# Kernel optimization log

Measured on AMD Instinct MI355X. Metric: run time of the kernel, lower is better.

Reference implementation:

```python
import jax, jax.numpy as jnp
import numpy as np

D, H, L, MLP = 1024, 16, 4, 4096
DH = D // H
EPS = 1e-5
SCALE_BASE = 512.0  # rotary_embedding_torch xpos default

def _ln(x, w, b):
    m = jnp.mean(x, axis=-1, keepdims=True)
    v = jnp.mean((x - m) ** 2, axis=-1, keepdims=True)
    return (x - m) * jax.lax.rsqrt(v + EPS) * w + b

def _rotate_half(x):
    # interleaved pair rotation: (x0, x1) -> (-x1, x0)
    x1, x2 = x[..., 0::2], x[..., 1::2]
    return jnp.stack((-x2, x1), axis=-1).reshape(x.shape)

def _rope_tables(S):
    inv = 1.0 / (10000.0 ** (jnp.arange(0, DH, 2, dtype=jnp.float32) / DH))
    pos = jnp.arange(S, dtype=jnp.float32)
    freqs = jnp.repeat(pos[:, None] * inv[None, :], 2, axis=-1)      # [S, DH]
    base = (jnp.arange(0, DH, 2, dtype=jnp.float32) + 0.4 * DH) / (1.4 * DH)
    power = (pos - S // 2) / SCALE_BASE
    scale = jnp.repeat(base[None, :] ** power[:, None], 2, axis=-1)  # [S, DH] xpos scale
    return jnp.cos(freqs), jnp.sin(freqs), scale

def setup_inputs() -> dict:
    key = jax.random.key(0)
    ks = jax.random.split(key, 8)
    B, S = 4, 1024
    w = 0.02
    return {
        "x": jax.random.normal(ks[0], (B, S, D), jnp.float32),
        "ln1_w": jnp.ones((L, D), jnp.float32), "ln1_b": jnp.zeros((L, D), jnp.float32),
        "wqkv": jax.random.normal(ks[1], (L, D, 3 * D), jnp.float32) * w,
        "bqkv": jnp.zeros((L, 3 * D), jnp.float32),
        "wo": jax.random.normal(ks[2], (L, D, D), jnp.float32) * w,
        "bo": jnp.zeros((L, D), jnp.float32),
        "ln2_w": jnp.ones((L, D), jnp.float32), "ln2_b": jnp.zeros((L, D), jnp.float32),
        "w1": jax.random.normal(ks[3], (L, D, MLP), jnp.float32) * w,
        "b1": jnp.zeros((L, MLP), jnp.float32),
        "w2": jax.random.normal(ks[4], (L, D, MLP), jnp.float32) * w,
        "b2": jnp.zeros((L, MLP), jnp.float32),
        "wout": jax.random.normal(ks[5], (L, MLP, D), jnp.float32) * w,
        "bout": jnp.zeros((L, D), jnp.float32),
        "fln_w": jnp.ones((D,), jnp.float32), "fln_b": jnp.zeros((D,), jnp.float32),
    }

def reference(x, ln1_w, ln1_b, wqkv, bqkv, wo, bo, ln2_w, ln2_b,
              w1, b1, w2, b2, wout, bout, fln_w, fln_b):
    B, S, _ = x.shape
    cos, sin, scale = _rope_tables(S)
    cos, sin, scale = cos[:, None, :], sin[:, None, :], scale[:, None, :]  # [S,1,DH] bcast heads
    inv_scale = 1.0 / scale
    attn_scale = DH ** -0.5
    for l in range(L):
        normed = _ln(x, ln1_w[l], ln1_b[l])
        qkv = (normed @ wqkv[l] + bqkv[l]).reshape(B, S, 3, H, DH)
        q, k, v = qkv[:, :, 0], qkv[:, :, 1], qkv[:, :, 2]  # [B,S,H,DH]
        q = (q * cos + _rotate_half(q) * sin) * scale       # xpos rotary, queries
        k = (k * cos + _rotate_half(k) * sin) * inv_scale   # xpos rotary, keys (scale**-1)
        attn = jnp.einsum('bihd,bjhd->bhij', q, k) * attn_scale
        attn = jax.nn.softmax(attn, axis=-1)
        y = jnp.einsum('bhij,bjhd->bihd', attn, v).reshape(B, S, D)
        x = x + y @ wo[l] + bo[l]
        h = _ln(x, ln2_w[l], ln2_b[l])
        ff = (jax.nn.silu(h @ w1[l] + b1[l]) * (h @ w2[l] + b2[l])) @ wout[l] + bout[l]
        x = x + ff
    return _ln(x, fln_w, fln_b)
```

## Files before the change

### kernel.cpp

```cpp
#include <hip/hip_runtime.h>
#include <hip/hip_bf16.h>
#include <math.h>


#define TD 1024
#define TH 16
#define TDH 64
#define TL 4
#define TMLP 4096
#define TB 4
#define TS 1024
#define TM (TB*TS)

typedef __attribute__((ext_vector_type(8))) short short8;
typedef __attribute__((ext_vector_type(4))) float f32x4;
typedef __attribute__((ext_vector_type(4))) unsigned short us4;
typedef __attribute__((ext_vector_type(2))) unsigned short us2;

__device__ __forceinline__ float bf2f(unsigned short u) {
  union { unsigned int i; float f; } x; x.i = ((unsigned int)u) << 16; return x.f;
}
__device__ __forceinline__ unsigned short f2bf(float f) {
  unsigned int x = __float_as_uint(f);
  unsigned int r = (x + 0x7FFFu + ((x >> 16) & 1u)) >> 16;
  return (unsigned short)r;
}

#if defined(__has_builtin)
#if __has_builtin(__builtin_amdgcn_global_load_lds)
#define TE_HAS_GLL 1
#endif
#endif

__device__ __forceinline__ void stage16(void* lds, const void* g) {
#ifdef TE_HAS_GLL
  __builtin_amdgcn_global_load_lds(
      (const __attribute__((address_space(1))) void*)g,
      (__attribute__((address_space(3))) void*)lds, 16, 0, 0);
#else
  *(short8*)lds = *(const short8*)g;
#endif
}

#define MFMA_BF16(a,b,c) __builtin_amdgcn_mfma_f32_16x16x32_bf16((a),(b),(c),0,0,0)

__global__ __launch_bounds__(256)
void te_tab(float4* __restrict__ tab) {
  int idx = blockIdx.x * 256 + threadIdx.x;
  int s = idx >> 5, i = idx & 31;
  float inv = powf(10000.0f, -(2.0f * (float)i) / 64.0f);
  float fr = (float)s * inv;
  float c = cosf(fr), sn = sinf(fr);
  float base = (2.0f * (float)i + 0.4f * 64.0f) / (1.4f * 64.0f);
  float p = ((float)s - 512.0f) / 512.0f;
  float scl = powf(base, p);
  float4 t;
  t.x = c; t.y = sn; t.z = scl * 0.125f; t.w = 1.0f / scl;
  tab[idx] = t;
}

__global__ __launch_bounds__(256)
void te_transpose_cvt(const float* __restrict__ src, unsigned short* __restrict__ dst,
                      int K, int N) {
  __shared__ float tile[32][33];
  int n0 = blockIdx.x * 32, k0 = blockIdx.y * 32;
  int tx = threadIdx.x, ty = threadIdx.y;
  #pragma unroll
  for (int j = 0; j < 4; ++j)
    tile[ty + 8*j][tx] = src[(size_t)(k0 + ty + 8*j) * N + n0 + tx];
  __syncthreads();
  #pragma unroll
  for (int j = 0; j < 4; ++j)
    dst[(size_t)(n0 + ty + 8*j) * K + k0 + tx] = f2bf(tile[tx][ty + 8*j]);
}

template<int OUTBF>
__global__ __launch_bounds__(256)
void te_ln(const float* __restrict__ in, const float* __restrict__ w,
           const float* __restrict__ b, void* __restrict__ outp) {
  int row = blockIdx.x, t = threadIdx.x;
  float4 v = ((const float4*)(in + (size_t)row * TD))[t];
  float s = v.x + v.y + v.z + v.w;
  float sq = v.x*v.x + v.y*v.y + v.z*v.z + v.w*v.w;
  #pragma unroll
  for (int o = 1; o < 64; o <<= 1) { s += __shfl_xor(s, o); sq += __shfl_xor(sq, o); }
  __shared__ float red[8];
  int wv = t >> 6;
  if ((t & 63) == 0) { red[wv] = s; red[4 + wv] = sq; }
  __syncthreads();
  s  = red[0] + red[1] + red[2] + red[3];
  sq = red[4] + red[5] + red[6] + red[7];
  float mean = s * (1.0f / TD);
  float rstd = rsqrtf(sq * (1.0f / TD) - mean * mean + 1e-5f);
  float4 w4 = ((const float4*)w)[t];
  float4 b4 = ((const float4*)b)[t];
  float r0 = (v.x - mean) * rstd * w4.x + b4.x;
  float r1 = (v.y - mean) * rstd * w4.y + b4.y;
  float r2 = (v.z - mean) * rstd * w4.z + b4.z;
  float r3 = (v.w - mean) * rstd * w4.w + b4.w;
  if (OUTBF) {
    us4 pk; pk[0] = f2bf(r0); pk[1] = f2bf(r1); pk[2] = f2bf(r2); pk[3] = f2bf(r3);
    ((us4*)outp)[(size_t)row * (TD/4) + t] = pk;
  } else {
    float4 o; o.x = r0; o.y = r1; o.z = r2; o.w = r3;
    ((float4*)outp)[(size_t)row * (TD/4) + t] = o;
  }
}

template<int MODE>
__global__ __launch_bounds__(256)
void te_gemm(const unsigned short* __restrict__ A, const unsigned short* __restrict__ Bt,
             const float* __restrict__ bias, const float* resid,
             const unsigned short* __restrict__ gate, void* outp,
             int M, int N, int K) {
  __shared__ short As[2][128 * 64];
  __shared__ short Bs[2][128 * 64];
  int bm = blockIdx.x, bn = blockIdx.y;
  int t = threadIdx.x;
  int lane = t & 63, w = t >> 6;
  int wr = w >> 1, wc = w & 1;
  int lr = lane & 15, lk = lane >> 4;
  f32x4 acc[4][4] = {};

  const short* Abase = (const short*)A + (size_t)(bm * 128) * K;
  const short* Bbase = (const short*)Bt + (size_t)(bn * 128) * K;
  int srow[4], scol[4];
  #pragma unroll
  for (int j = 0; j < 4; ++j) {
    int m = j * 256 + t;
    int r = m >> 3, c = m & 7;
    srow[j] = r;
    scol[j] = (c ^ (r & 7)) * 8;
  }

  auto stage_tile = [&](int buf, int k0) {
    #pragma unroll
    for (int j = 0; j < 4; ++j) {
      stage16(&As[buf][j * 2048 + t * 8], Abase + (size_t)srow[j] * K + k0 + scol[j]);
      stage16(&Bs[buf][j * 2048 + t * 8], Bbase + (size_t)srow[j] * K + k0 + scol[j]);
    }
  };

  auto compute_tile = [&](int buf) {
    #pragma unroll
    for (int ks = 0; ks < 2; ++ks) {
      short8 af[4], bfv[4];
      #pragma unroll
      for (int mi = 0; mi < 4; ++mi) {
        int row = wr * 64 + mi * 16 + lr;
        int cc = (ks * 4 + lk) ^ (row & 7);
        af[mi] = *(const short8*)&As[buf][row * 64 + cc * 8];
      }
      #pragma unroll
      for (int nj = 0; nj < 4; ++nj) {
        int row = wc * 64 + nj * 16 + lr;
        int cc = (ks * 4 + lk) ^ (row & 7);
        bfv[nj] = *(const short8*)&Bs[buf][row * 64 + cc * 8];
      }
      #pragma unroll
      for (int mi = 0; mi < 4; ++mi)
        #pragma unroll
        for (int nj = 0; nj < 4; ++nj)
          acc[mi][nj] = MFMA_BF16(af[mi], bfv[nj], acc[mi][nj]);
    }
  };

  int nk = K >> 6;
  stage_tile(0, 0);
  __syncthreads();
  int cur = 0;
  for (int kt = 0; kt < nk; ++kt) {
    if (kt + 1 < nk) stage_tile(cur ^ 1, (kt + 1) << 6);
    compute_tile(cur);
    __syncthreads();
    cur ^= 1;
  }

  #pragma unroll
  for (int mi = 0; mi < 4; ++mi) {
    #pragma unroll
    for (int nj = 0; nj < 4; ++nj) {
      int col = bn*128 + wc*64 + nj*16 + lr;
      float bv = bias[col];
      #pragma unroll
      for (int r = 0; r < 4; ++r) {
        int row = bm*128 + wr*64 + mi*16 + lk*4 + r;
        size_t o = (size_t)row * N + col;
        float val = acc[mi][nj][r] + bv;
        if (MODE == 0) {
          ((unsigned short*)outp)[o] = f2bf(val);
        } else if (MODE == 1) {
          ((float*)outp)[o] = resid[o] + val;
        } else {
          float a = bf2f(gate[o]);
          float sg = a / (1.0f + __expf(-a));
          ((unsigned short*)outp)[o] = f2bf(sg * val);
        }
      }
    }
  }
}

__global__ __launch_bounds__(256)
void te_rope(const unsigned short* __restrict__ qkv, const float4* __restrict__ tab,
             unsigned short* __restrict__ qb, unsigned short* __restrict__ kb) {
  int idx = blockIdx.x * 256 + threadIdx.x;
  int i = idx & 31;
  int h = (idx >> 5) & 15;
  int row = idx >> 9;
  int s = row & (TS - 1);
  float4 t4 = tab[(s << 5) + i];
  size_t base = (size_t)row * (3*TD) + h * TDH + 2*i;
  us2 qp = *(const us2*)&qkv[base];
  us2 kp = *(const us2*)&qkv[base + TD];
  float qe = bf2f(qp[0]), qo = bf2f(qp[1]);
  float ke = bf2f(kp[0]), ko = bf2f(kp[1]);
  size_t ob = (size_t)row * TD + h * TDH + 2*i;
  us2 qo2, ko2;
  qo2[0] = f2bf((qe * t4.x - qo * t4.y) * t4.z);
  qo2[1] = f2bf((qo * t4.x + qe * t4.y) * t4.z);
  ko2[0] = f2bf((ke * t4.x - ko * t4.y) * t4.w);
  ko2[1] = f2bf((ko * t4.x + ke * t4.y) * t4.w);
  *(us2*)&qb[ob] = qo2;
  *(us2*)&kb[ob] = ko2;
}

__global__ __launch_bounds__(256)
void te_attn(const unsigned short* __restrict__ qb, const unsigned short* __restrict__ kb,
             const unsigned short* __restrict__ qkv, unsigned short* __restrict__ y) {
  __shared__ char Ks[8192];
  __shared__ char Vs[8192];
  __shared__ char Ps[4][2048];
  int qt = blockIdx.x;
  int bh = blockIdx.y;
  int b = bh >> 4, h = bh & 15;
  int t = threadIdx.x, lane = t & 63, w = t >> 6;
  int lq = lane & 15, lg = lane >> 4;

  const unsigned short* vptr = qkv + 2*TD;

  int qrow = b*TS + qt*64 + w*16 + lq;
  short8 aq0 = *(const short8*)&qb[(size_t)qrow*TD + h*TDH + lg*8];
  short8 aq1 = *(const short8*)&qb[(size_t)qrow*TD + h*TDH + 32 + lg*8];

  f32x4 oacc[4] = {};
  float rm[4] = {-3e38f, -3e38f, -3e38f, -3e38f};
  float rl[4] = {0.f, 0.f, 0.f, 0.f};

  int srr = t >> 3;
  int scb = (t & 7) * 8;

  for (int kt = 0; kt < TS/64; ++kt) {
    int kbase = b*TS + kt*64;
    __syncthreads();
    #pragma unroll
    for (int half = 0; half < 2; ++half) {
      int row = srr + half*32;
      short8 d = *(const short8*)&kb[(size_t)(kbase + row)*TD + h*TDH + scb];
      int off = (row*128 + scb*2) ^ ((row & 7) << 4);
      *(short8*)&Ks[off] = d;
    }
    #pragma unroll
    for (int half = 0; half < 2; ++half) {
      int dh = srr + half*32;
      short8 d;
      #pragma unroll
      for (int i = 0; i < 8; ++i)
        d[i] = (short)vptr[(size_t)(kbase + scb + i)*(3*TD) + h*TDH + dh];
      int off = (dh*128 + scb*2) ^ ((dh & 7) << 4);
      *(short8*)&Vs[off] = d;
    }
    __syncthreads();
    f32x4 sc[4];
    #pragma unroll
    for (int nj = 0; nj < 4; ++nj) {
      int row = nj*16 + lq;
      int sw = (row & 7) << 4;
      short8 b0 = *(const short8*)&Ks[(row*128 + lg*16) ^ sw];
      short8 b1 = *(const short8*)&Ks[(row*128 + 64 + lg*16) ^ sw];
      f32x4 c = {};
      c = MFMA_BF16(aq0, b0, c);
      c = MFMA_BF16(aq1, b1, c);
      sc[nj] = c;
    }
    float mn[4], al[4];
    #pragma unroll
    for (int r = 0; r < 4; ++r) {
      float x = fmaxf(fmaxf(sc[0][r], sc[1][r]), fmaxf(sc[2][r], sc[3][r]));
      #pragma unroll
      for (int o = 1; o < 16; o <<= 1) x = fmaxf(x, __shfl_xor(x, o));
      mn[r] = fmaxf(rm[r], x);
      al[r] = __expf(rm[r] - mn[r]);
      rm[r] = mn[r];
    }
    #pragma unroll
    for (int nj = 0; nj < 4; ++nj)
      #pragma unroll
      for (int r = 0; r < 4; ++r)
        sc[nj][r] = __expf(sc[nj][r] - mn[r]);
    #pragma unroll
    for (int r = 0; r < 4; ++r) {
      float x = sc[0][r] + sc[1][r] + sc[2][r] + sc[3][r];
      #pragma unroll
      for (int o = 1; o < 16; o <<= 1) x += __shfl_xor(x, o);
      rl[r] = rl[r] * al[r] + x;
    }
    #pragma unroll
    for (int d0 = 0; d0 < 4; ++d0)
      #pragma unroll
      for (int r = 0; r < 4; ++r)
        oacc[d0][r] *= al[r];
    #pragma unroll
    for (int nj = 0; nj < 4; ++nj)
      #pragma unroll
      for (int r = 0; r < 4; ++r) {
        int row = lg*4 + r;
        int off = (row*128 + (nj*16 + lq)*2) ^ ((row & 7) << 4);
        *(short*)&Ps[w][off] = (short)f2bf(sc[nj][r]);
      }
    short8 pa0, pa1;
    {
      int sw = (lq & 7) << 4;
      pa0 = *(const short8*)&Ps[w][(lq*128 + lg*16) ^ sw];
      pa1 = *(const short8*)&Ps[w][(lq*128 + 64 + lg*16) ^ sw];
    }
    #pragma unroll
    for (int d0 = 0; d0 < 4; ++d0) {
      int row = d0*16 + lq;
      int sw = (row & 7) << 4;
      short8 b0 = *(const short8*)&Vs[(row*128 + lg*16) ^ sw];
      short8 b1 = *(const short8*)&Vs[(row*128 + 64 + lg*16) ^ sw];
      oacc[d0] = MFMA_BF16(pa0, b0, oacc[d0]);
      oacc[d0] = MFMA_BF16(pa1, b1, oacc[d0]);
    }
  }
  #pragma unroll
  for (int d0 = 0; d0 < 4; ++d0)
    #pragma unroll
    for (int r = 0; r < 4; ++r) {
      int row = b*TS + qt*64 + w*16 + lg*4 + r;
      float val = oacc[d0][r] / rl[r];
      y[(size_t)row*TD + h*TDH + d0*16 + lq] = f2bf(val);
    }
}

extern "C" void kernel_launch(void* const* d_in, const int* in_sizes, int n_in,
                              void* d_out, int out_size, void* d_ws, size_t ws_size,
                              hipStream_t stream) {
  const float* x_in = (const float*)d_in[0];
  const float* ln1w = (const float*)d_in[1];
  const float* ln1b = (const float*)d_in[2];
  const float* wqkv = (const float*)d_in[3];
  const float* bqkv = (const float*)d_in[4];
  const float* wo   = (const float*)d_in[5];
  const float* bo   = (const float*)d_in[6];
  const float* ln2w = (const float*)d_in[7];
  const float* ln2b = (const float*)d_in[8];
  const float* w1   = (const float*)d_in[9];
  const float* b1   = (const float*)d_in[10];
  const float* w2   = (const float*)d_in[11];
  const float* b2   = (const float*)d_in[12];
  const float* wout = (const float*)d_in[13];
  const float* bout = (const float*)d_in[14];
  const float* flnw = (const float*)d_in[15];
  const float* flnb = (const float*)d_in[16];

  char* ws = (char*)d_ws;
  size_t off = 0;
  auto alloc = [&](size_t bytes) -> void* {
    void* p = ws + off;
    off += (bytes + 255) & ~(size_t)255;
    return p;
  };
  unsigned short* wqkv_t = (unsigned short*)alloc((size_t)3*TD*TD*2);
  unsigned short* wo_t   = (unsigned short*)alloc((size_t)TD*TD*2);
  unsigned short* w1_t   = (unsigned short*)alloc((size_t)TMLP*TD*2);
  unsigned short* w2_t   = (unsigned short*)alloc((size_t)TMLP*TD*2);
  unsigned short* wout_t = (unsigned short*)alloc((size_t)TD*TMLP*2);
  float*          x      = (float*)alloc((size_t)TM*TD*4);
  unsigned short* nrm    = (unsigned short*)alloc((size_t)TM*TD*2);
  unsigned short* u1     = (unsigned short*)alloc((size_t)TM*TMLP*2);
  unsigned short* qbuf   = (unsigned short*)alloc((size_t)TM*TD*2);
  unsigned short* kbuf   = (unsigned short*)alloc((size_t)TM*TD*2);
  unsigned short* u2     = (unsigned short*)alloc((size_t)TM*TMLP*2);
  float4*         tab    = (float4*)alloc((size_t)TS*32*sizeof(float4));

  dim3 blk256(256);
  dim3 tblk(32, 8);
  te_tab<<<dim3(TS*32/256), blk256, 0, stream>>>(tab);
  hipMemcpyAsync(x, x_in, (size_t)TM*TD*4, hipMemcpyDeviceToDevice, stream);

  for (int l = 0; l < TL; ++l) {
    te_transpose_cvt<<<dim3(3*TD/32, TD/32), tblk, 0, stream>>>(
        wqkv + (size_t)l*TD*3*TD, wqkv_t, TD, 3*TD);
    te_transpose_cvt<<<dim3(TD/32, TD/32), tblk, 0, stream>>>(
        wo + (size_t)l*TD*TD, wo_t, TD, TD);
    te_transpose_cvt<<<dim3(TMLP/32, TD/32), tblk, 0, stream>>>(
        w1 + (size_t)l*TD*TMLP, w1_t, TD, TMLP);
    te_transpose_cvt<<<dim3(TMLP/32, TD/32), tblk, 0, stream>>>(
        w2 + (size_t)l*TD*TMLP, w2_t, TD, TMLP);
    te_transpose_cvt<<<dim3(TD/32, TMLP/32), tblk, 0, stream>>>(
        wout + (size_t)l*TMLP*TD, wout_t, TMLP, TD);

    te_ln<1><<<dim3(TM), blk256, 0, stream>>>(x, ln1w + l*TD, ln1b + l*TD, nrm);
    te_gemm<0><<<dim3(TM/128, 3*TD/128), blk256, 0, stream>>>(
        nrm, wqkv_t, bqkv + l*3*TD, nullptr, nullptr, u1, TM, 3*TD, TD);
    te_rope<<<dim3(TM*TH*32/256), blk256, 0, stream>>>(u1, tab, qbuf, kbuf);
    te_attn<<<dim3(TS/64, TB*TH), blk256, 0, stream>>>(qbuf, kbuf, u1, u2);
    te_gemm<1><<<dim3(TM/128, TD/128), blk256, 0, stream>>>(
        u2, wo_t, bo + l*TD, x, nullptr, x, TM, TD, TD);
    te_ln<1><<<dim3(TM), blk256, 0, stream>>>(x, ln2w + l*TD, ln2b + l*TD, nrm);
    te_gemm<0><<<dim3(TM/128, TMLP/128), blk256, 0, stream>>>(
        nrm, w1_t, b1 + l*TMLP, nullptr, nullptr, u1, TM, TMLP, TD);
    te_gemm<2><<<dim3(TM/128, TMLP/128), blk256, 0, stream>>>(
        nrm, w2_t, b2 + l*TMLP, nullptr, u1, u2, TM, TMLP, TD);
    te_gemm<1><<<dim3(TM/128, TD/128), blk256, 0, stream>>>(
        u2, wout_t, bout + l*TD, x, nullptr, x, TM, TD, TMLP);
  }
  te_ln<0><<<dim3(TM), blk256, 0, stream>>>(x, flnw, flnb, (float*)d_out);

  (void)in_sizes; (void)n_in; (void)out_size; (void)ws_size;
}
```

Measured before the change: 1.726 ms.

## Fuse gated MLP GEMMs, pre-transpose V, pipeline attention K/V loads, use exp2

Interleaves w1 and w2 weights into one transposed buffer so a single 256x256-tile, 512-thread GEMM computes both projections and applies SiLU gating in its epilogue. This removes the separate u1 write and re-read and the second pass over the normalized activations. V is transposed into a per-head buffer by a new kernel, so attention can load K and V with double-buffered async LDS staging instead of strided scalar gathers. Attention blocks are remapped to group heads per XCD, and softmax uses exp2 with log2(e) folded into the query scale. The cost is an extra transpose kernel, plus higher LDS and register pressure in the larger GEMM tile.

```diff
diff --git a/kernel.cpp b/kernel.cpp
--- a/kernel.cpp
+++ b/kernel.cpp
@@ -11,6 +11,8 @@
 #define TB 4
 #define TS 1024
 #define TM (TB*TS)
+
+#define LOG2E 1.4426950408889634f
 
 typedef __attribute__((ext_vector_type(8))) short short8;
 typedef __attribute__((ext_vector_type(4))) float f32x4;
@@ -55,7 +57,7 @@
   float p = ((float)s - 512.0f) / 512.0f;
   float scl = powf(base, p);
   float4 t;
-  t.x = c; t.y = sn; t.z = scl * 0.125f; t.w = 1.0f / scl;
+  t.x = c; t.y = sn; t.z = scl * 0.125f * LOG2E; t.w = 1.0f / scl;
   tab[idx] = t;
 }
 
@@ -72,6 +74,43 @@
   #pragma unroll
   for (int j = 0; j < 4; ++j)
     dst[(size_t)(n0 + ty + 8*j) * K + k0 + tx] = f2bf(tile[tx][ty + 8*j]);
+}
+
+__global__ __launch_bounds__(256)
+void te_transpose_cvt2(const float* __restrict__ src1, const float* __restrict__ src2,
+                       unsigned short* __restrict__ dst, int K, int N) {
+  __shared__ float tile[32][33];
+  const float* src = blockIdx.z ? src2 : src1;
+  int part = blockIdx.z;
+  int n0 = blockIdx.x * 32, k0 = blockIdx.y * 32;
+  int tx = threadIdx.x, ty = threadIdx.y;
+  #pragma unroll
+  for (int j = 0; j < 4; ++j)
+    tile[ty + 8*j][tx] = src[(size_t)(k0 + ty + 8*j) * N + n0 + tx];
+  __syncthreads();
+  #pragma unroll
+  for (int j = 0; j < 4; ++j) {
+    int n = n0 + ty + 8*j;
+    int R = ((n >> 4) << 5) + part * 16 + (n & 15);
+    dst[(size_t)R * K + k0 + tx] = f2bf(tile[tx][ty + 8*j]);
+  }
+}
+
+__global__ __launch_bounds__(256)
+void te_vt(const unsigned short* __restrict__ qkv, unsigned short* __restrict__ vt) {
+  __shared__ unsigned short tile[32][34];
+  int s0 = blockIdx.x * 32, c0 = blockIdx.y * 32, b = blockIdx.z;
+  int tx = threadIdx.x, ty = threadIdx.y;
+  #pragma unroll
+  for (int j = 0; j < 4; ++j)
+    tile[ty + 8*j][tx] = qkv[(size_t)(b*TS + s0 + ty + 8*j) * (3*TD) + 2*TD + c0 + tx];
+  __syncthreads();
+  #pragma unroll
+  for (int j = 0; j < 4; ++j) {
+    int col = c0 + ty + 8*j;
+    vt[(size_t)(b*TH + (col >> 6)) * (TDH*TS) + (size_t)(col & 63) * TS + s0 + tx] =
+        tile[tx][ty + 8*j];
+  }
 }
 
 template<int OUTBF>
@@ -191,11 +230,91 @@
           ((unsigned short*)outp)[o] = f2bf(val);
         } else if (MODE == 1) {
           ((float*)outp)[o] = resid[o] + val;
-        } else {
-          float a = bf2f(gate[o]);
-          float sg = a / (1.0f + __expf(-a));
-          ((unsigned short*)outp)[o] = f2bf(sg * val);
         }
+      }
+    }
+  }
+  (void)gate;
+}
+
+__global__ __launch_bounds__(512)
+void te_gemm_mlp(const unsigned short* __restrict__ A, const unsigned short* __restrict__ Bt,
+                 const float* __restrict__ b1p, const float* __restrict__ b2p,
+                 unsigned short* __restrict__ outp, int K) {
+  __shared__ short As[2][256 * 32];
+  __shared__ short Bs[2][256 * 32];
+  int bm = blockIdx.x, bn = blockIdx.y;
+  int t = threadIdx.x;
+  int lane = t & 63, w = t >> 6;
+  int wr = w >> 2, wc = w & 3;
+  int lr = lane & 15, lk = lane >> 4;
+  f32x4 acc[8][4] = {};
+
+  const short* Abase = (const short*)A + (size_t)(bm * 256) * K;
+  const short* Bbase = (const short*)Bt + (size_t)(bn * 256) * K;
+  int srow[2], scol[2];
+  #pragma unroll
+  for (int j = 0; j < 2; ++j) {
+    int m = j * 512 + t;
+    int r = m >> 2, c = m & 3;
+    srow[j] = r;
+    scol[j] = (c ^ (r & 3)) * 8;
+  }
+
+  auto stage_tile = [&](int buf, int k0) {
+    #pragma unroll
+    for (int j = 0; j < 2; ++j) {
+      stage16(&As[buf][j * 4096 + t * 8], Abase + (size_t)srow[j] * K + k0 + scol[j]);
+      stage16(&Bs[buf][j * 4096 + t * 8], Bbase + (size_t)srow[j] * K + k0 + scol[j]);
+    }
+  };
+
+  auto compute_tile = [&](int buf) {
+    short8 af[8], bfv[4];
+    #pragma unroll
+    for (int mi = 0; mi < 8; ++mi) {
+      int row = wr * 128 + mi * 16 + lr;
+      int cc = lk ^ (row & 3);
+      af[mi] = *(const short8*)&As[buf][row * 32 + cc * 8];
+    }
+    #pragma unroll
+    for (int nj = 0; nj < 4; ++nj) {
+      int row = wc * 64 + nj * 16 + lr;
+      int cc = lk ^ (row & 3);
+      bfv[nj] = *(const short8*)&Bs[buf][row * 32 + cc * 8];
+    }
+    #pragma unroll
+    for (int mi = 0; mi < 8; ++mi)
+      #pragma unroll
+      for (int nj = 0; nj < 4; ++nj)
+        acc[mi][nj] = MFMA_BF16(af[mi], bfv[nj], acc[mi][nj]);
+  };
+
+  int nk = K >> 5;
+  stage_tile(0, 0);
+  __syncthreads();
+  int cur = 0;
+  for (int kt = 0; kt < nk; ++kt) {
+    if (kt + 1 < nk) stage_tile(cur ^ 1, (kt + 1) << 5);
+    compute_tile(cur);
+    __syncthreads();
+    cur ^= 1;
+  }
+
+  #pragma unroll
+  for (int mi = 0; mi < 8; ++mi) {
+    #pragma unroll
+    for (int njp = 0; njp < 2; ++njp) {
+      int mcol = bn*128 + wc*32 + njp*16 + lr;
+      float bva = b1p[mcol];
+      float bvg = b2p[mcol];
+      #pragma unroll
+      for (int r = 0; r < 4; ++r) {
+        int row = bm*256 + wr*128 + mi*16 + lk*4 + r;
+        float a = acc[mi][njp*2][r] + bva;
+        float g = acc[mi][njp*2+1][r] + bvg;
+        float sg = a / (1.0f + __expf(-a));
+        outp[(size_t)row * TMLP + mcol] = f2bf(sg * g);
       }
     }
   }
@@ -227,57 +346,61 @@
 
 __global__ __launch_bounds__(256)
 void te_attn(const unsigned short* __restrict__ qb, const unsigned short* __restrict__ kb,
-             const unsigned short* __restrict__ qkv, unsigned short* __restrict__ y) {
-  __shared__ char Ks[8192];
-  __shared__ char Vs[8192];
+             const unsigned short* __restrict__ vt, unsigned short* __restrict__ y) {
+  __shared__ short Ks[2][64 * 64];
+  __shared__ short Vs[2][64 * 64];
   __shared__ char Ps[4][2048];
-  int qt = blockIdx.x;
-  int bh = blockIdx.y;
+  int bid = blockIdx.x;
+  int xcd = bid & 7, j = bid >> 3;
+  int qt = j & 15;
+  int bh = (j >> 4) * 8 + xcd;
   int b = bh >> 4, h = bh & 15;
   int t = threadIdx.x, lane = t & 63, w = t >> 6;
   int lq = lane & 15, lg = lane >> 4;
 
-  const unsigned short* vptr = qkv + 2*TD;
-
   int qrow = b*TS + qt*64 + w*16 + lq;
   short8 aq0 = *(const short8*)&qb[(size_t)qrow*TD + h*TDH + lg*8];
   short8 aq1 = *(const short8*)&qb[(size_t)qrow*TD + h*TDH + 32 + lg*8];
 
+  const unsigned short* kbase_p = kb + (size_t)(b*TS) * TD + h * TDH;
+  const unsigned short* vbase_p = vt + (size_t)bh * (TDH*TS);
+
   f32x4 oacc[4] = {};
   float rm[4] = {-3e38f, -3e38f, -3e38f, -3e38f};
   float rl[4] = {0.f, 0.f, 0.f, 0.f};
 
-  int srr = t >> 3;
-  int scb = (t & 7) * 8;
-
+  int srow[2], scol[2];
+  #pragma unroll
+  for (int j2 = 0; j2 < 2; ++j2) {
+    int m = j2 * 256 + t;
+    int r = m >> 3, c = m & 7;
+    srow[j2] = r;
+    scol[j2] = (c ^ (r & 7)) * 8;
+  }
+
+  auto stage_kv = [&](int buf, int kt) {
+    int s0 = kt * 64;
+    #pragma unroll
+    for (int j2 = 0; j2 < 2; ++j2) {
+      stage16(&Ks[buf][j2 * 2048 + t * 8],
+              kbase_p + (size_t)(s0 + srow[j2]) * TD + scol[j2]);
+      stage16(&Vs[buf][j2 * 2048 + t * 8],
+              vbase_p + (size_t)srow[j2] * TS + s0 + scol[j2]);
+    }
+  };
+
+  stage_kv(0, 0);
+  __syncthreads();
+  int cur = 0;
   for (int kt = 0; kt < TS/64; ++kt) {
-    int kbase = b*TS + kt*64;
-    __syncthreads();
-    #pragma unroll
-    for (int half = 0; half < 2; ++half) {
-      int row = srr + half*32;
-      short8 d = *(const short8*)&kb[(size_t)(kbase + row)*TD + h*TDH + scb];
-      int off = (row*128 + scb*2) ^ ((row & 7) << 4);
-      *(short8*)&Ks[off] = d;
-    }
-    #pragma unroll
-    for (int half = 0; half < 2; ++half) {
-      int dh = srr + half*32;
-      short8 d;
-      #pragma unroll
-      for (int i = 0; i < 8; ++i)
-        d[i] = (short)vptr[(size_t)(kbase + scb + i)*(3*TD) + h*TDH + dh];
-      int off = (dh*128 + scb*2) ^ ((dh & 7) << 4);
-      *(short8*)&Vs[off] = d;
-    }
-    __syncthreads();
+    if (kt + 1 < TS/64) stage_kv(cur ^ 1, kt + 1);
     f32x4 sc[4];
     #pragma unroll
     for (int nj = 0; nj < 4; ++nj) {
       int row = nj*16 + lq;
-      int sw = (row & 7) << 4;
-      short8 b0 = *(const short8*)&Ks[(row*128 + lg*16) ^ sw];
-      short8 b1 = *(const short8*)&Ks[(row*128 + 64 + lg*16) ^ sw];
+      int sw = (row & 7);
+      short8 b0 = *(const short8*)&Ks[cur][row * 64 + (lg ^ sw) * 8];
+      short8 b1 = *(const short8*)&Ks[cur][row * 64 + ((4 + lg) ^ sw) * 8];
       f32x4 c = {};
       c = MFMA_BF16(aq0, b0, c);
       c = MFMA_BF16(aq1, b1, c);
@@ -290,14 +413,14 @@
       #pragma unroll
       for (int o = 1; o < 16; o <<= 1) x = fmaxf(x, __shfl_xor(x, o));
       mn[r] = fmaxf(rm[r], x);
-      al[r] = __expf(rm[r] - mn[r]);
+      al[r] = exp2f(rm[r] - mn[r]);
       rm[r] = mn[r];
     }
     #pragma unroll
     for (int nj = 0; nj < 4; ++nj)
       #pragma unroll
       for (int r = 0; r < 4; ++r)
-        sc[nj][r] = __expf(sc[nj][r] - mn[r]);
+        sc[nj][r] = exp2f(sc[nj][r] - mn[r]);
     #pragma unroll
     for (int r = 0; r < 4; ++r) {
       float x = sc[0][r] + sc[1][r] + sc[2][r] + sc[3][r];
@@ -327,12 +450,14 @@
     #pragma unroll
     for (int d0 = 0; d0 < 4; ++d0) {
       int row = d0*16 + lq;
-      int sw = (row & 7) << 4;
-      short8 b0 = *(const short8*)&Vs[(row*128 + lg*16) ^ sw];
-      short8 b1 = *(const short8*)&Vs[(row*128 + 64 + lg*16) ^ sw];
+      int sw = (row & 7);
+      short8 b0 = *(const short8*)&Vs[cur][row * 64 + (lg ^ sw) * 8];
+      short8 b1 = *(const short8*)&Vs[cur][row * 64 + ((4 + lg) ^ sw) * 8];
       oacc[d0] = MFMA_BF16(pa0, b0, oacc[d0]);
       oacc[d0] = MFMA_BF16(pa1, b1, oacc[d0]);
     }
+    __syncthreads();
+    cur ^= 1;
   }
   #pragma unroll
   for (int d0 = 0; d0 < 4; ++d0)
@@ -374,8 +499,7 @@
   };
   unsigned short* wqkv_t = (unsigned short*)alloc((size_t)3*TD*TD*2);
   unsigned short* wo_t   = (unsigned short*)alloc((size_t)TD*TD*2);
-  unsigned short* w1_t   = (unsigned short*)alloc((size_t)TMLP*TD*2);
-  unsigned short* w2_t   = (unsigned short*)alloc((size_t)TMLP*TD*2);
+  unsigned short* w12_t  = (unsigned short*)alloc((size_t)2*TMLP*TD*2);
   unsigned short* wout_t = (unsigned short*)alloc((size_t)TD*TMLP*2);
   float*          x      = (float*)alloc((size_t)TM*TD*4);
   unsigned short* nrm    = (unsigned short*)alloc((size_t)TM*TD*2);
@@ -384,6 +508,7 @@
   unsigned short* kbuf   = (unsigned short*)alloc((size_t)TM*TD*2);
   unsigned short* u2     = (unsigned short*)alloc((size_t)TM*TMLP*2);
   float4*         tab    = (float4*)alloc((size_t)TS*32*sizeof(float4));
+  unsigned short* vtbuf  = u2 + (size_t)TM*TD;
 
   dim3 blk256(256);
   dim3 tblk(32, 8);
@@ -395,10 +520,8 @@
         wqkv + (size_t)l*TD*3*TD, wqkv_t, TD, 3*TD);
     te_transpose_cvt<<<dim3(TD/32, TD/32), tblk, 0, stream>>>(
         wo + (size_t)l*TD*TD, wo_t, TD, TD);
-    te_transpose_cvt<<<dim3(TMLP/32, TD/32), tblk, 0, stream>>>(
-        w1 + (size_t)l*TD*TMLP, w1_t, TD, TMLP);
-    te_transpose_cvt<<<dim3(TMLP/32, TD/32), tblk, 0, stream>>>(
-        w2 + (size_t)l*TD*TMLP, w2_t, TD, TMLP);
+    te_transpose_cvt2<<<dim3(TMLP/32, TD/32, 2), tblk, 0, stream>>>(
+        w1 + (size_t)l*TD*TMLP, w2 + (size_t)l*TD*TMLP, w12_t, TD, TMLP);
     te_transpose_cvt<<<dim3(TD/32, TMLP/32), tblk, 0, stream>>>(
         wout + (size_t)l*TMLP*TD, wout_t, TMLP, TD);
 
@@ -406,14 +529,13 @@
     te_gemm<0><<<dim3(TM/128, 3*TD/128), blk256, 0, stream>>>(
         nrm, wqkv_t, bqkv + l*3*TD, nullptr, nullptr, u1, TM, 3*TD, TD);
     te_rope<<<dim3(TM*TH*32/256), blk256, 0, stream>>>(u1, tab, qbuf, kbuf);
-    te_attn<<<dim3(TS/64, TB*TH), blk256, 0, stream>>>(qbuf, kbuf, u1, u2);
+    te_vt<<<dim3(TS/32, TD/32, TB), tblk, 0, stream>>>(u1, vtbuf);
+    te_attn<<<dim3(TB*TH*(TS/64)), blk256, 0, stream>>>(qbuf, kbuf, vtbuf, u2);
     te_gemm<1><<<dim3(TM/128, TD/128), blk256, 0, stream>>>(
         u2, wo_t, bo + l*TD, x, nullptr, x, TM, TD, TD);
     te_ln<1><<<dim3(TM), blk256, 0, stream>>>(x, ln2w + l*TD, ln2b + l*TD, nrm);
-    te_gemm<0><<<dim3(TM/128, TMLP/128), blk256, 0, stream>>>(
-        nrm, w1_t, b1 + l*TMLP, nullptr, nullptr, u1, TM, TMLP, TD);
-    te_gemm<2><<<dim3(TM/128, TMLP/128), blk256, 0, stream>>>(
-        nrm, w2_t, b2 + l*TMLP, nullptr, u1, u2, TM, TMLP, TD);
+    te_gemm_mlp<<<dim3(TM/256, 2*TMLP/256), dim3(512), 0, stream>>>(
+        nrm, w12_t, b1 + l*TMLP, b2 + l*TMLP, u2, TD);
     te_gemm<1><<<dim3(TM/128, TD/128), blk256, 0, stream>>>(
         u2, wout_t, bout + l*TD, x, nullptr, x, TM, TD, TMLP);
   }
```

Measured after the change: 1.589 ms. -7.9%, faster.
